# Kernel optimization log

Measured on AMD Instinct MI355X. Metric: run time of the kernel, lower is better.

Reference implementation:

```python
import jax, jax.numpy as jnp
import numpy as np

HIDDEN = 256

def setup_inputs() -> dict:
    key = jax.random.key(0)
    k1, k2, k3, k4, k5 = jax.random.split(key, 5)
    B, T, I, H = 1024, 336, 64, HIDDEN
    s = 1.0 / np.sqrt(H)  # PyTorch LSTM init scale
    return {
        "x": jax.random.normal(k1, (B, T, I), dtype=jnp.float32),
        "W_ih": jax.random.uniform(k2, (4 * H, I), dtype=jnp.float32, minval=-s, maxval=s),
        "W_hh": jax.random.uniform(k3, (4 * H, H), dtype=jnp.float32, minval=-s, maxval=s),
        "b_ih": jax.random.uniform(k4, (4 * H,), dtype=jnp.float32, minval=-s, maxval=s),
        "b_hh": jax.random.uniform(k5, (4 * H,), dtype=jnp.float32, minval=-s, maxval=s),
    }

def reference(x, W_ih, W_hh, b_ih, b_hh):
    # Single-layer unidirectional LSTM (batch_first), PyTorch gate order i,f,g,o.
    B, T, I = x.shape
    H = W_hh.shape[1]
    # Precompute input contribution for all timesteps: [T, B, 4H]
    x_gates = jnp.einsum('bti,gi->tbg', x, W_ih) + (b_ih + b_hh)

    def step(carry, xg_t):
        h, c = carry
        gates = xg_t + h @ W_hh.T          # [B, 4H]
        i, f, g, o = jnp.split(gates, 4, axis=-1)
        c_new = jax.nn.sigmoid(f) * c + jax.nn.sigmoid(i) * jnp.tanh(g)
        h_new = jax.nn.sigmoid(o) * jnp.tanh(c_new)
        return (h_new, c_new), None

    h0 = jnp.zeros((B, H), dtype=x.dtype)
    c0 = jnp.zeros((B, H), dtype=x.dtype)
    (hT, cT), _ = jax.lax.scan(step, (h0, c0), x_gates)
    # hn, cn shaped [num_layers*D, B, H] = [1, B, H]
    return hT[None], cT[None]
```

## Files before the change

kernel.cpp:

```cpp
#include <hip/hip_runtime.h>
#include <cstdint>


#define NGROUP  64
#define BATCH_G 16
#define T_STEPS 336
#define I_DIM   64
#define H_DIM   256
#define VSTRIDE 336
#define PAIRS   128
#define OUT_HALF 262144

typedef __attribute__((ext_vector_type(8))) __bf16 bf16x8;
typedef __attribute__((ext_vector_type(8))) unsigned short ushort8_t;
typedef __attribute__((ext_vector_type(4))) float f32x4;
typedef __attribute__((ext_vector_type(4))) unsigned uint32x4;
typedef __attribute__((ext_vector_type(2))) unsigned uint32x2;

__device__ inline unsigned short f2bf(float f) {
  unsigned u = __builtin_bit_cast(unsigned, f);
  return (unsigned short)((u + 0x7fffu + ((u >> 16) & 1u)) >> 16);
}
__device__ inline float sigf(float x) { return 1.f / (1.f + __expf(-x)); }
__device__ inline float tanhfast(float x) { return 1.f - 2.f / (1.f + __expf(2.f * x)); }

__device__ inline void ld2_tagged(const uint32x2* p, uint32x4& a, uint32x4& b) {
  asm volatile(
      "global_load_dwordx4 %0, %2, off sc0 sc1\n\t"
      "global_load_dwordx4 %1, %3, off sc0 sc1\n\t"
      "s_waitcnt vmcnt(0)"
      : "=&v"(a), "=&v"(b)
      : "v"(p), "v"(p + 2)
      : "memory");
}
__device__ inline void st_pair(uint32x2* p, uint32x2 v) {
  asm volatile("global_store_dwordx2 %0, %1, off sc0 sc1" :: "v"(p), "v"(v) : "memory");
}

__device__ inline void stage_h(const uint32x2* hsrc, unsigned tag, unsigned short* hdst) {
  uint32x4 A, Bv;
  int it = 0;
  for (;;) {
    ld2_tagged(hsrc, A, Bv);
    bool ok = (A[0] == tag) & (A[2] == tag) & (Bv[0] == tag) & (Bv[2] == tag);
    if (ok) break;
    if (++it > (1 << 17)) break;
    __builtin_amdgcn_s_sleep(1);
  }
  *(unsigned*)(hdst + 0 * VSTRIDE) = A[1];
  *(unsigned*)(hdst + 1 * VSTRIDE) = A[3];
  *(unsigned*)(hdst + 2 * VSTRIDE) = Bv[1];
  *(unsigned*)(hdst + 3 * VSTRIDE) = Bv[3];
}

__global__ __launch_bounds__(512, 2) void lstm_persistent(
    const float* __restrict__ x, const float* __restrict__ W_ih,
    const float* __restrict__ W_hh, const float* __restrict__ b_ih,
    const float* __restrict__ b_hh, float* __restrict__ out,
    uint32x2* __restrict__ hbuf)
{
  __shared__ __align__(16) unsigned short v_lds[2][BATCH_G * VSTRIDE];

  const int tid  = threadIdx.x;
  const int gid  = blockIdx.x & 63;
  const int mid  = blockIdx.x >> 6;
  const int wv   = tid >> 6;
  const int l    = tid & 63;
  const int l15  = l & 15, quad = l >> 4;
  const int rg   = wv;

  bf16x8 afrag[2][10];
#pragma unroll
  for (int rt = 0; rt < 2; ++rt) {
    int grow = (l15 & 3) * H_DIM + mid * 64 + rg * 8 + rt * 4 + (l15 >> 2);
    const float* wih_row = W_ih + (long)grow * I_DIM;
    const float* whh_row = W_hh + (long)grow * H_DIM;
#pragma unroll
    for (int kt = 0; kt < 10; ++kt) {
      int kbase = kt * 32 + quad * 8;
      ushort8_t a;
#pragma unroll
      for (int e = 0; e < 8; ++e) {
        int k = kbase + e;
        float v = (k < I_DIM) ? wih_row[k] : whh_row[k - I_DIM];
        a[e] = f2bf(v);
      }
      afrag[rt][kt] = __builtin_bit_cast(bf16x8, a);
    }
  }

  f32x4 bias[2];
#pragma unroll
  for (int rt = 0; rt < 2; ++rt) {
#pragma unroll
    for (int g = 0; g < 4; ++g) {
      int grow = g * H_DIM + mid * 64 + rg * 8 + rt * 4 + quad;
      bias[rt][g] = b_ih[grow] + b_hh[grow];
    }
  }

  const int batch = l15;
  float c_reg[2] = {0.f, 0.f};
  float h_keep[2];

  const int b_stage = tid >> 5;
  const int x_i2    = (tid & 31) * 2;
  const float* xrow = x + ((long)(gid * BATCH_G + b_stage)) * T_STEPS * I_DIM + x_i2;

  const int p_ld  = tid >> 2;
  const int b0_ld = (tid & 3) * 4;
  const uint32x2* ld_base = hbuf + ((long)gid * PAIRS + p_ld) * BATCH_G + b0_ld;

  uint32x2* st_base = hbuf + ((long)gid * PAIRS + mid * 32 + rg * 4 + (quad >> 1)) * BATCH_G + batch;
  const long buf_stride = (long)NGROUP * PAIRS * BATCH_G;
  const bool own_wave = ((wv >> 1) == mid);

  float2 xv = *(const float2*)xrow;

  for (int t = 1; t <= T_STEPS; ++t) {
    unsigned short* vbuf = v_lds[t & 1];

    {
      ushort2 xb;
      xb.x = f2bf(xv.x); xb.y = f2bf(xv.y);
      *(ushort2*)&vbuf[b_stage * VSTRIDE + x_i2] = xb;
    }
    if (t < T_STEPS) xv = *(const float2*)(xrow + (long)t * I_DIM);

    unsigned short* hdst = vbuf + b0_ld * VSTRIDE + I_DIM + 2 * p_ld;
    if (t > 1) {
      if (!own_wave) {
        const unsigned tag = (unsigned)(t - 1);
        const uint32x2* hsrc = ld_base + ((t - 1) & 1) * buf_stride;
        stage_h(hsrc, tag, hdst);
      }
    } else {
#pragma unroll
      for (int j = 0; j < 4; ++j) *(unsigned*)(hdst + j * VSTRIDE) = 0u;
    }
    __syncthreads();

    f32x4 acc0 = bias[0], acc1 = bias[1];
    const unsigned short* vb = vbuf + (unsigned)batch * VSTRIDE + quad * 8;
#pragma unroll
    for (int kt = 0; kt < 10; ++kt) {
      bf16x8 bv = __builtin_bit_cast(bf16x8, *(const uint32x4*)(vb + kt * 32));
      acc0 = __builtin_amdgcn_mfma_f32_16x16x32_bf16(afrag[0][kt], bv, acc0, 0, 0, 0);
      acc1 = __builtin_amdgcn_mfma_f32_16x16x32_bf16(afrag[1][kt], bv, acc1, 0, 0, 0);
    }

    __builtin_amdgcn_s_setprio(1);
    unsigned short* next_own = v_lds[(t + 1) & 1] + batch * VSTRIDE + I_DIM + mid * 64;
#pragma unroll
    for (int rt = 0; rt < 2; ++rt) {
      const f32x4 acc = rt ? acc1 : acc0;
      float c = sigf(acc[1]) * c_reg[rt] + sigf(acc[0]) * tanhfast(acc[2]);
      float h = sigf(acc[3]) * tanhfast(c);
      c_reg[rt] = c; h_keep[rt] = h;
      unsigned short hb16 = f2bf(h);
      next_own[rg * 8 + rt * 4 + quad] = hb16;
      unsigned hb = (unsigned)hb16;
      unsigned partner = (unsigned)__shfl_xor((int)hb, 16, 64);
      if (!(quad & 1)) {
        uint32x2 pv;
        pv[0] = (unsigned)t;
        pv[1] = hb | (partner << 16);
        st_pair(st_base + rt * 2 * BATCH_G + (t & 1) * buf_stride, pv);
      }
    }
    __builtin_amdgcn_s_setprio(0);
  }

#pragma unroll
  for (int rt = 0; rt < 2; ++rt) {
    int gcol = mid * 64 + rg * 8 + rt * 4 + quad;
    long o = (long)(gid * BATCH_G + batch) * H_DIM + gcol;
    out[o]            = h_keep[rt];
    out[OUT_HALF + o] = c_reg[rt];
  }
}

extern "C" void kernel_launch(void* const* d_in, const int* in_sizes, int n_in,
                              void* d_out, int out_size, void* d_ws, size_t ws_size,
                              hipStream_t stream) {
  const float* x    = (const float*)d_in[0];
  const float* W_ih = (const float*)d_in[1];
  const float* W_hh = (const float*)d_in[2];
  const float* b_ih = (const float*)d_in[3];
  const float* b_hh = (const float*)d_in[4];
  float* out = (float*)d_out;

  uint32x2* hbuf = (uint32x2*)d_ws;

  hipMemsetAsync(d_ws, 0, 2u * NGROUP * PAIRS * BATCH_G * 8u, stream);
  lstm_persistent<<<dim3(256), dim3(512), 0, stream>>>(x, W_ih, W_hh, b_ih, b_hh, out, hbuf);
}
```

Measured before the change: 916.5 us.

## Overlap own-block h and x MFMAs with remote h polling

Result: faster. 789.3 us (-13.9%).

```diff
diff --git a/kernel.cpp b/kernel.cpp
--- a/kernel.cpp
+++ b/kernel.cpp
@@ -23,6 +23,12 @@
 }
 __device__ inline float sigf(float x) { return 1.f / (1.f + __expf(-x)); }
 __device__ inline float tanhfast(float x) { return 1.f - 2.f / (1.f + __expf(2.f * x)); }
+
+__device__ inline int slot_kt(int s, int mid) {
+  return (s < 2) ? s
+       : (s < 4) ? (2 + 2 * mid + (s - 2))
+       : (((s - 4) < 2 * mid) ? (s - 2) : s);
+}
 
 __device__ inline void ld2_tagged(const uint32x2* p, uint32x4& a, uint32x4& b) {
   asm volatile(
@@ -76,7 +82,8 @@
     const float* wih_row = W_ih + (long)grow * I_DIM;
     const float* whh_row = W_hh + (long)grow * H_DIM;
 #pragma unroll
-    for (int kt = 0; kt < 10; ++kt) {
+    for (int s = 0; s < 10; ++s) {
+      int kt = slot_kt(s, mid);
       int kbase = kt * 32 + quad * 8;
       ushort8_t a;
 #pragma unroll
@@ -85,7 +92,7 @@
         float v = (k < I_DIM) ? wih_row[k] : whh_row[k - I_DIM];
         a[e] = f2bf(v);
       }
-      afrag[rt][kt] = __builtin_bit_cast(bf16x8, a);
+      afrag[rt][s] = __builtin_bit_cast(bf16x8, a);
     }
   }
 
@@ -114,6 +121,12 @@
   uint32x2* st_base = hbuf + ((long)gid * PAIRS + mid * 32 + rg * 4 + (quad >> 1)) * BATCH_G + batch;
   const long buf_stride = (long)NGROUP * PAIRS * BATCH_G;
   const bool own_wave = ((wv >> 1) == mid);
+
+  {
+    int zr = tid >> 5, zc = (tid & 31) * 8;
+    uint32x4 z = {0u, 0u, 0u, 0u};
+    *(uint32x4*)&v_lds[1][zr * VSTRIDE + I_DIM + zc] = z;
+  }
 
   float2 xv = *(const float2*)xrow;
 
@@ -127,26 +140,31 @@
     }
     if (t < T_STEPS) xv = *(const float2*)(xrow + (long)t * I_DIM);
 
-    unsigned short* hdst = vbuf + b0_ld * VSTRIDE + I_DIM + 2 * p_ld;
-    if (t > 1) {
-      if (!own_wave) {
-        const unsigned tag = (unsigned)(t - 1);
-        const uint32x2* hsrc = ld_base + ((t - 1) & 1) * buf_stride;
-        stage_h(hsrc, tag, hdst);
-      }
-    } else {
-#pragma unroll
-      for (int j = 0; j < 4; ++j) *(unsigned*)(hdst + j * VSTRIDE) = 0u;
-    }
     __syncthreads();
 
     f32x4 acc0 = bias[0], acc1 = bias[1];
     const unsigned short* vb = vbuf + (unsigned)batch * VSTRIDE + quad * 8;
 #pragma unroll
-    for (int kt = 0; kt < 10; ++kt) {
+    for (int s = 0; s < 4; ++s) {
+      int kt = slot_kt(s, mid);
       bf16x8 bv = __builtin_bit_cast(bf16x8, *(const uint32x4*)(vb + kt * 32));
-      acc0 = __builtin_amdgcn_mfma_f32_16x16x32_bf16(afrag[0][kt], bv, acc0, 0, 0, 0);
-      acc1 = __builtin_amdgcn_mfma_f32_16x16x32_bf16(afrag[1][kt], bv, acc1, 0, 0, 0);
+      acc0 = __builtin_amdgcn_mfma_f32_16x16x32_bf16(afrag[0][s], bv, acc0, 0, 0, 0);
+      acc1 = __builtin_amdgcn_mfma_f32_16x16x32_bf16(afrag[1][s], bv, acc1, 0, 0, 0);
+    }
+
+    if (t > 1 && !own_wave) {
+      unsigned short* hdst = vbuf + b0_ld * VSTRIDE + I_DIM + 2 * p_ld;
+      const uint32x2* hsrc = ld_base + ((t - 1) & 1) * buf_stride;
+      stage_h(hsrc, (unsigned)(t - 1), hdst);
+    }
+    __syncthreads();
+
+#pragma unroll
+    for (int s = 4; s < 10; ++s) {
+      int kt = slot_kt(s, mid);
+      bf16x8 bv = __builtin_bit_cast(bf16x8, *(const uint32x4*)(vb + kt * 32));
+      acc0 = __builtin_amdgcn_mfma_f32_16x16x32_bf16(afrag[0][s], bv, acc0, 0, 0, 0);
+      acc1 = __builtin_amdgcn_mfma_f32_16x16x32_bf16(afrag[1][s], bv, acc1, 0, 0, 0);
     }
 
     __builtin_amdgcn_s_setprio(1);
```
